# Optimization experiments

Measured on AMD Instinct MI355X. Metric: run time of the kernel, lower is better.

Reference implementation:

```python
import jax, jax.numpy as jnp
import numpy as np

N = 8192
TOKEN_DIM = 384
K = 16
D_IN = 2 * (TOKEN_DIM + 3)  # 774


def setup_inputs() -> dict:
    key = jax.random.key(0)
    k1, k2, k3, k4, k5, k6 = jax.random.split(key, 6)
    xyz = jax.random.normal(k1, (N, 3), dtype=jnp.float32)
    feat = jax.random.normal(k2, (N, TOKEN_DIM), dtype=jnp.float32)
    W1 = jax.random.normal(k3, (D_IN, TOKEN_DIM), dtype=jnp.float32) / np.sqrt(D_IN)
    b1 = jax.random.normal(k4, (TOKEN_DIM,), dtype=jnp.float32) * 0.01
    W2 = jax.random.normal(k5, (TOKEN_DIM, 3), dtype=jnp.float32) / np.sqrt(TOKEN_DIM)
    b2 = jax.random.normal(k6, (3,), dtype=jnp.float32) * 0.01
    return {"xyz": xyz, "feat": feat, "W1": W1, "b1": b1, "W2": W2, "b2": b2}


def _knn_idx(xyz, k):
    # pairwise squared distances [N, N]; loop=False -> exclude self via +inf diag
    sq = jnp.sum(xyz * xyz, axis=-1)
    d2 = sq[:, None] + sq[None, :] - 2.0 * (xyz @ xyz.T)
    n = xyz.shape[0]
    d2 = jnp.where(jnp.eye(n, dtype=bool), jnp.inf, d2)
    _, idx = jax.lax.top_k(-d2, k)  # idx[i] = k nearest neighbors (sources) of target i
    return idx


def reference(xyz, feat, W1, b1, W2, b2):
    idx = _knn_idx(xyz, K)                      # [N, K] int32
    x = jnp.concatenate([feat, xyz], axis=-1)   # [N, D] with D = token_dim + 3
    x_j = x[idx]                                # [N, K, D] gathered neighbor feats
    x_i = x[:, None, :]                         # [N, 1, D]
    # EdgeConv message: nn(cat([x_i, x_j - x_i]))
    e = jnp.concatenate([jnp.broadcast_to(x_i, x_j.shape), x_j - x_i], axis=-1)  # [N, K, 2D]
    h = jax.nn.relu(jnp.einsum('nkd,df->nkf', e, W1) + b1)   # [N, K, token_dim]
    m = jnp.einsum('nkf,fo->nko', h, W2) + b2                # [N, K, 3]
    agg = jnp.max(m, axis=1)                                 # max aggregation over neighbors
    return xyz + agg
```

## Files before the change

kernel.cpp:

```cpp
#include <hip/hip_runtime.h>
#include <hip/hip_bf16.h>


#define N 8192
#define TD 384
#define KNN 16
#define DX 387
#define KP 416
#define NF 768
#define INFF __builtin_inff()

#define NB_X (N/2)
#define NB_W NF
#define NB_A 32
#define NGEMM_T 1536

typedef __attribute__((ext_vector_type(8))) short short8;
typedef __attribute__((ext_vector_type(4))) float f32x4;
typedef __attribute__((ext_vector_type(2))) float f32x2;


__device__ __forceinline__ f32x2 pk_mul(f32x2 a, f32x2 b) {
    f32x2 r; asm("v_pk_mul_f32 %0, %1, %2" : "=v"(r) : "v"(a), "v"(b)); return r;
}
__device__ __forceinline__ f32x2 pk_add(f32x2 a, f32x2 b) {
    f32x2 r; asm("v_pk_add_f32 %0, %1, %2" : "=v"(r) : "v"(a), "v"(b)); return r;
}
__device__ __forceinline__ f32x2 pk_sub(f32x2 a, f32x2 b) {
    f32x2 r; asm("v_pk_add_f32 %0, %1, %2 neg_lo:[0,1] neg_hi:[0,1]" : "=v"(r) : "v"(a), "v"(b)); return r;
}
__device__ __forceinline__ f32x2 pk_fma(f32x2 a, f32x2 b, f32x2 c) {
    f32x2 r; asm("v_pk_fma_f32 %0, %1, %2, %3" : "=v"(r) : "v"(a), "v"(b), "v"(c)); return r;
}

__device__ __forceinline__ void dist4(f32x2 qx, f32x2 qy, f32x2 qz, f32x2 qw,
                                      f32x2 x01, f32x2 x23, f32x2 y01, f32x2 y23,
                                      f32x2 z01, f32x2 z23, f32x2 s01, f32x2 s23,
                                      f32x2& d01, f32x2& d23) {
    f32x2 dot01 = pk_fma(qz, z01, pk_fma(qy, y01, pk_mul(qx, x01)));
    f32x2 dot23 = pk_fma(qz, z23, pk_fma(qy, y23, pk_mul(qx, x23)));
    d01 = pk_sub(pk_add(qw, s01), pk_add(dot01, dot01));
    d23 = pk_sub(pk_add(qw, s23), pk_add(dot23, dot23));
}

__device__ __forceinline__ int xbin(float x) {
    int b = (int)((x + 4.0f) * 32.0f);
    return b < 0 ? 0 : (b > 255 ? 255 : b);
}

__device__ __forceinline__ float rdlane_f(float v, int src) {
    return __uint_as_float(__builtin_amdgcn_readlane(__float_as_uint(v), src));
}
__device__ __forceinline__ unsigned udmap(float x) {
    unsigned u = __float_as_uint(x);
    return ((int)u < 0) ? ~u : (u | 0x80000000u);
}


__global__ void __launch_bounds__(256) prep_assign(const float* __restrict__ feat,
                                                   const float* __restrict__ xyz,
                                                   const float* __restrict__ W1,
                                                   __hip_bfloat16* __restrict__ Xb,
                                                   __hip_bfloat16* __restrict__ Wpt,
                                                   int* __restrict__ tlo,
                                                   int* __restrict__ thi,
                                                   float* __restrict__ stile) {
    const int b = blockIdx.x;
    const int t = threadIdx.x;
    if (b < NB_X) {
        const int half = t >> 7;
        const int tt = t & 127;
        const int p = b*2 + half;
        if (tt < 96) {
            float4 f = reinterpret_cast<const float4*>(feat + (size_t)p*TD)[tt];
            __hip_bfloat16 h[4] = {__float2bfloat16(f.x), __float2bfloat16(f.y),
                                   __float2bfloat16(f.z), __float2bfloat16(f.w)};
            *reinterpret_cast<ulonglong1*>(Xb + p*KP + tt*4) = *reinterpret_cast<ulonglong1*>(h);
        } else {
            int d = TD + (tt - 96);
            float v = (d < DX) ? xyz[p*3 + (d - TD)] : 0.f;
            Xb[p*KP + d] = __float2bfloat16(v);
        }
        return;
    }
    if (b < NB_X + NB_W) {
        const int f = b - NB_X;
        for (int k = t; k < KP; k += 256) {
            float v = 0.f;
            if (k < DX) {
                if (f < TD) v = W1[k*TD + f] - W1[(DX+k)*TD + f];
                else        v = W1[(DX+k)*TD + (f - TD)];
            }
            Wpt[f*KP + k] = __float2bfloat16(v);
        }
        return;
    }

    __shared__ int hcnt[256], pre[256], scan[256], cur[256];
    __shared__ int stlo[32], sthi[32];
    const int a = b - (NB_X + NB_W);
    hcnt[t] = 0; pre[t] = 0; cur[t] = 0;
    if (t < 32) { stlo[t] = 255; sthi[t] = 0; }
    __syncthreads();

    #pragma unroll
    for (int c = 0; c < 32; ++c) {
        int bin = xbin(xyz[(c*256 + t)*3]);
        atomicAdd(&hcnt[bin], 1);
        if (c < a) atomicAdd(&pre[bin], 1);
    }
    __syncthreads();

    const int v = hcnt[t];
    scan[t] = v;
    __syncthreads();
    for (int off = 1; off < 256; off <<= 1) {
        int add = (t >= off) ? scan[t - off] : 0;
        __syncthreads();
        scan[t] += add;
        __syncthreads();
    }
    const int end = scan[t], start = end - v;
    if (a == 0 && v > 0) {
        for (int x = start >> 8; x <= (end - 1) >> 8; ++x) {
            atomicMin(&stlo[x], t);
            atomicMax(&sthi[x], t);
        }
    }
    __syncthreads();
    scan[t] = start;
    __syncthreads();
    if (a == 0 && t < 32) { tlo[t] = stlo[t]; thi[t] = sthi[t]; }

    const int i = a*256 + t;
    float x = xyz[i*3+0], y = xyz[i*3+1], z = xyz[i*3+2];
    int bin = xbin(x);
    int pos = scan[bin] + pre[bin] + atomicAdd(&cur[bin], 1);
    float sq = __fadd_rn(__fadd_rn(__fmul_rn(x,x), __fmul_rn(y,y)), __fmul_rn(z,z));
    float* tp = stile + (pos >> 8) * 1280 + (pos & 255);
    tp[0] = x; tp[256] = y; tp[512] = z; tp[768] = sq;
    reinterpret_cast<int*>(tp)[1024] = i;
}


__global__ void __launch_bounds__(64) knn_gemm(const float* __restrict__ stile,
                                               const int* __restrict__ tlo,
                                               const int* __restrict__ thi,
                                               int* __restrict__ knn,
                                               const __hip_bfloat16* __restrict__ Xb,
                                               const __hip_bfloat16* __restrict__ Wpt,
                                               const float* __restrict__ b1,
                                               __hip_bfloat16* __restrict__ Ub,
                                               __hip_bfloat16* __restrict__ Vb) {
    __shared__ unsigned sbuf[128][2];
    const int u = blockIdx.x;
    const int g = u / 6;
    const int r = u - g*6;
    const int lane = threadIdx.x;

    if ((r == 5) && (g < NGEMM_T)) {
        const int i0  = (g & 127) * 64;
        const int f0  = (g >> 7) * 64;
        const int lm  = lane & 15;
        const int lk  = (lane >> 4) * 8;

        f32x4 acc[4][4];
        #pragma unroll
        for (int rr = 0; rr < 4; ++rr)
            #pragma unroll
            for (int c = 0; c < 4; ++c)
                acc[rr][c] = (f32x4){0.f, 0.f, 0.f, 0.f};

        const __hip_bfloat16* xbase = Xb  + (size_t)(i0 + lm) * KP + lk;
        const __hip_bfloat16* wbase = Wpt + (size_t)(f0 + lm) * KP + lk;

        #pragma unroll
        for (int kk = 0; kk < 13; ++kk) {
            short8 aa[4], bb[4];
            #pragma unroll
            for (int rr = 0; rr < 4; ++rr)
                aa[rr] = *reinterpret_cast<const short8*>(xbase + (size_t)rr*16*KP + kk*32);
            #pragma unroll
            for (int c = 0; c < 4; ++c)
                bb[c] = *reinterpret_cast<const short8*>(wbase + (size_t)c*16*KP + kk*32);
            #pragma unroll
            for (int rr = 0; rr < 4; ++rr)
                #pragma unroll
                for (int c = 0; c < 4; ++c)
                    acc[rr][c] = __builtin_amdgcn_mfma_f32_16x16x32_bf16(aa[rr], bb[c], acc[rr][c], 0, 0, 0);
        }

        const bool isU = (f0 < TD);
        __hip_bfloat16* outb = isU ? (Ub + f0) : (Vb + (f0 - TD));
        float bias[4] = {0.f, 0.f, 0.f, 0.f};
        if (isU) {
            #pragma unroll
            for (int c = 0; c < 4; ++c) bias[c] = b1[f0 + c*16 + lm];
        }
        const int crow = (lane >> 4) * 4;
        #pragma unroll
        for (int rr = 0; rr < 4; ++rr)
            #pragma unroll
            for (int c = 0; c < 4; ++c)
                #pragma unroll
                for (int q = 0; q < 4; ++q)
                    outb[(size_t)(i0 + rr*16 + crow + q) * TD + c*16 + lm] =
                        __float2bfloat16(acc[rr][c][q] + bias[c]);
        return;
    }

    const int s  = u - ((g < NGEMM_T) ? g : NGEMM_T);
    const int tq   = s >> 8;
    const int sl   = (s & 255) >> 2;
    const int slot = s & 3;

    const float* qp = stile + tq*1280 + (s & 255);
    const float qx = qp[0], qy = qp[256], qz = qp[512], qw = qp[768];
    const int   qi = reinterpret_cast<const int*>(qp)[1024];
    const f32x2 qx2 = {qx,qx}, qy2 = {qy,qy}, qz2 = {qz,qz}, qw2 = {qw,qw};

    const float* lbase = stile + lane*4;
    const bool is_self_lane = (lane == sl);

    int lo = tq - 2; if (lo < 0) lo = 0; if (lo > 27) lo = 27;
    float4 X[5], Y[5], Z[5], S[5];
    int4   I[5];
    #pragma unroll
    for (int tt = 0; tt < 5; ++tt) {
        const float* tp = lbase + (lo + tt)*1280;
        X[tt] = *(const float4*)(tp);
        Y[tt] = *(const float4*)(tp + 256);
        Z[tt] = *(const float4*)(tp + 512);
        S[tt] = *(const float4*)(tp + 768);
        I[tt] = *(const int4*)(tp + 1024);
    }
    __builtin_amdgcn_sched_barrier(0);

    float dd[5][4];
    float mn = INFF;
    #pragma unroll
    for (int tt = 0; tt < 5; ++tt) {
        const int t = lo + tt;
        f32x2 x01 = {X[tt].x, X[tt].y}, x23 = {X[tt].z, X[tt].w};
        f32x2 y01 = {Y[tt].x, Y[tt].y}, y23 = {Y[tt].z, Y[tt].w};
        f32x2 z01 = {Z[tt].x, Z[tt].y}, z23 = {Z[tt].z, Z[tt].w};
        f32x2 s01 = {S[tt].x, S[tt].y}, s23 = {S[tt].z, S[tt].w};
        f32x2 d01, d23;
        dist4(qx2, qy2, qz2, qw2, x01, x23, y01, y23, z01, z23, s01, s23, d01, d23);
        if ((t == tq) && is_self_lane) {
            if      (slot == 0) d01[0] = INFF;
            else if (slot == 1) d01[1] = INFF;
            else if (slot == 2) d23[0] = INFF;
            else                d23[1] = INFF;
        }
        dd[tt][0] = d01[0]; dd[tt][1] = d01[1];
        dd[tt][2] = d23[0]; dd[tt][3] = d23[1];
        mn = fminf(mn, fminf(fminf(d01[0], d01[1]), fminf(d23[0], d23[1])));
    }

    float T;
    {
        unsigned ub = udmap(mn);
        unsigned long long alive = ~0ull;
        int need = KNN;
        for (int b = 31; b >= 0; --b) {
            if (__popcll(alive) == 1) break;
            unsigned long long ones  = __ballot(((ub >> b) & 1u) != 0u);
            unsigned long long zeros = alive & ~ones;
            int cz = (int)__popcll(zeros);
            bool tz = (cz >= need);
            alive = tz ? zeros : (alive & ones);
            need  = tz ? need : (need - cz);
        }
        T = fmaxf(rdlane_f(mn, (int)__ffsll(alive) - 1), 0.f);
    }

    unsigned mask;
    {
        const int ti = lane & 31;
        const int bl = tlo[ti], bh = thi[ti];
        const float xlo = (bl == 0)   ? -1e30f : (bl * 0.03125f - 4.0f);
        const float xhi = (bh == 255) ?  1e30f : ((bh + 1) * 0.03125f - 4.0f);
        float gap = fmaxf(0.f, fmaxf(xlo - qx, qx - xhi));
        bool gate = (gap * gap <= T + 1e-3f);
        mask = (unsigned)__ballot(gate && (lane < 32));
    }

    int cnt = 0;
    const unsigned long long ltm = (1ull << lane) - 1;

    auto push = [&](float dv, int idx) {
        bool pred = (dv <= T);
        unsigned long long bal = __ballot(pred);
        if (bal) {
            int posn = cnt + (int)__popcll(bal & ltm);
            if (pred && posn < 128) {
                sbuf[posn][0] = udmap(dv);
                sbuf[posn][1] = (unsigned)idx;
            }
            cnt += (int)__popcll(bal);
        }
    };

    #pragma unroll
    for (int tt = 0; tt < 5; ++tt) {
        const int t = lo + tt;
        if (!((mask >> t) & 1u)) continue;
        push(dd[tt][0], I[tt].x);
        push(dd[tt][1], I[tt].y);
        push(dd[tt][2], I[tt].z);
        push(dd[tt][3], I[tt].w);
    }
    unsigned rest = mask & ~(0x1Fu << lo);
    while (rest) {
        const int t = (int)__ffs(rest) - 1;
        rest &= rest - 1;
        const float* tp = lbase + t*1280;
        float4 Xr = *(const float4*)(tp);
        float4 Yr = *(const float4*)(tp + 256);
        float4 Zr = *(const float4*)(tp + 512);
        float4 Sr = *(const float4*)(tp + 768);
        int4   Ir = *(const int4*)(tp + 1024);
        f32x2 x01 = {Xr.x,Xr.y}, x23 = {Xr.z,Xr.w};
        f32x2 y01 = {Yr.x,Yr.y}, y23 = {Yr.z,Yr.w};
        f32x2 z01 = {Zr.x,Zr.y}, z23 = {Zr.z,Zr.w};
        f32x2 s01 = {Sr.x,Sr.y}, s23 = {Sr.z,Sr.w};
        f32x2 d01, d23;
        dist4(qx2, qy2, qz2, qw2, x01, x23, y01, y23, z01, z23, s01, s23, d01, d23);
        float tmin = fminf(fminf(d01[0], d01[1]), fminf(d23[0], d23[1]));
        if (__ballot(tmin <= T)) {
            push(d01[0], Ir.x);
            push(d01[1], Ir.y);
            push(d23[0], Ir.z);
            push(d23[1], Ir.w);
        }
    }

    asm volatile("s_waitcnt lgkmcnt(0)" ::: "memory");
    const int M = (cnt > 128) ? 128 : cnt;

    if (M <= 64) {
        unsigned ud1 = 0xFFFFFFFFu, id1 = 0xFFFFFFFFu;
        if (lane < M) { ud1 = sbuf[lane][0]; id1 = sbuf[lane][1]; }
        unsigned long long alive = __ballot(lane < M);
        int need = KNN;
        for (int b = 31; b >= 0; --b) {
            if (__popcll(alive) == 1) break;
            unsigned long long on = __ballot(((ud1 >> b) & 1u) != 0u);
            unsigned long long z  = alive & ~on;
            int cz = (int)__popcll(z);
            bool tz = (cz >= need);
            alive = tz ? z : (alive & on);
            need  = tz ? need : (need - cz);
        }
        unsigned v16 = (unsigned)__builtin_amdgcn_readlane((int)ud1, (int)__ffsll(alive) - 1);
        const bool all_ties = ((int)__popcll(alive) <= need);
        unsigned vidx = 0xFFFFFFFFu;
        if (!all_ties) {
            unsigned long long a = alive;
            int nd = need;
            for (int b = 31; b >= 0; --b) {
                if (__popcll(a) == 1) break;
                unsigned long long on = __ballot(((id1 >> b) & 1u) != 0u);
                unsigned long long z  = a & ~on;
                int cz = (int)__popcll(z);
                bool tz = (cz >= nd);
                a  = tz ? z : (a & on);
                nd = tz ? nd : (nd - cz);
            }
            vidx = (unsigned)__builtin_amdgcn_readlane((int)id1, (int)__ffsll(a) - 1);
        }
        bool sel = (lane < M) && ((ud1 < v16) || ((ud1 == v16) && (all_ties || (id1 <= vidx))));
        unsigned long long bs = __ballot(sel);
        if (sel) knn[qi*KNN + (int)__popcll(bs & ltm)] = (int)id1;
    } else {
        unsigned ud1 = 0xFFFFFFFFu, id1 = 0xFFFFFFFFu;
        unsigned ud2 = 0xFFFFFFFFu, id2 = 0xFFFFFFFFu;
        if (lane < M)      { ud1 = sbuf[lane][0];      id1 = sbuf[lane][1]; }
        if (lane + 64 < M) { ud2 = sbuf[lane + 64][0]; id2 = sbuf[lane + 64][1]; }

        unsigned long long alive1 = __ballot(lane < M);
        unsigned long long alive2 = __ballot(lane + 64 < M);
        int need = KNN;
        for (int b = 31; b >= 0; --b) {
            if ((int)__popcll(alive1) + (int)__popcll(alive2) == 1) break;
            unsigned long long on1 = __ballot(((ud1 >> b) & 1u) != 0u);
            unsigned long long on2 = __ballot(((ud2 >> b) & 1u) != 0u);
            unsigned long long z1 = alive1 & ~on1;
            unsigned long long z2 = alive2 & ~on2;
            int cz = (int)__popcll(z1) + (int)__popcll(z2);
            bool tz = (cz >= need);
            alive1 = tz ? z1 : (alive1 & on1);
            alive2 = tz ? z2 : (alive2 & on2);
            need   = tz ? need : (need - cz);
        }
        unsigned v16;
        if (alive1) v16 = (unsigned)__builtin_amdgcn_readlane((int)ud1, (int)__ffsll(alive1) - 1);
        else        v16 = (unsigned)__builtin_amdgcn_readlane((int)ud2, (int)__ffsll(alive2) - 1);

        const int nt = (int)__popcll(alive1) + (int)__popcll(alive2);
        const bool all_ties = (nt <= need);
        unsigned vidx = 0xFFFFFFFFu;
        if (!all_ties) {
            unsigned long long a1 = alive1, a2 = alive2;
            int nd = need;
            for (int b = 31; b >= 0; --b) {
                if ((int)__popcll(a1) + (int)__popcll(a2) == 1) break;
                unsigned long long on1 = __ballot(((id1 >> b) & 1u) != 0u);
                unsigned long long on2 = __ballot(((id2 >> b) & 1u) != 0u);
                unsigned long long z1 = a1 & ~on1;
                unsigned long long z2 = a2 & ~on2;
                int cz = (int)__popcll(z1) + (int)__popcll(z2);
                bool tz = (cz >= nd);
                a1 = tz ? z1 : (a1 & on1);
                a2 = tz ? z2 : (a2 & on2);
                nd = tz ? nd : (nd - cz);
            }
            if (a1) vidx = (unsigned)__builtin_amdgcn_readlane((int)id1, (int)__ffsll(a1) - 1);
            else    vidx = (unsigned)__builtin_amdgcn_readlane((int)id2, (int)__ffsll(a2) - 1);
        }

        bool sel1 = (lane < M)      && ((ud1 < v16) || ((ud1 == v16) && (all_ties || (id1 <= vidx))));
        bool sel2 = (lane + 64 < M) && ((ud2 < v16) || ((ud2 == v16) && (all_ties || (id2 <= vidx))));
        unsigned long long bs1 = __ballot(sel1);
        if (sel1) knn[qi*KNN + (int)__popcll(bs1 & ltm)] = (int)id1;
        const int c1 = (int)__popcll(bs1);
        unsigned long long bs2 = __ballot(sel2);
        if (sel2) knn[qi*KNN + c1 + (int)__popcll(bs2 & ltm)] = (int)id2;
    }
}


__device__ __forceinline__ float bflo(unsigned w) { return __uint_as_float(w << 16); }
__device__ __forceinline__ float bfhi(unsigned w) { return __uint_as_float(w & 0xFFFF0000u); }

template<int CTRL>
__device__ __forceinline__ float dppf(float v) {
    return __uint_as_float((unsigned)__builtin_amdgcn_update_dpp(
        0, (int)__float_as_uint(v), CTRL, 0xF, 0xF, true));
}

__global__ void __launch_bounds__(256) final_kernel(const __hip_bfloat16* __restrict__ Ub,
                                                    const __hip_bfloat16* __restrict__ Vb,
                                                    const int* __restrict__ knn,
                                                    const float* __restrict__ xyz,
                                                    const float* __restrict__ W2,
                                                    const float* __restrict__ b2,
                                                    float* __restrict__ out) {
    const int lane = threadIdx.x & 63;
    const int wv   = threadIdx.x >> 6;
    const int i    = blockIdx.x * 4 + wv;
    const int d0   = lane * 6;

    int jreg = knn[i*KNN + (lane & 15)];

    float u[6], w2l[6][3];
    {
        const unsigned* rowU = reinterpret_cast<const unsigned*>(Ub + (size_t)i * TD) + lane*3;
        unsigned a0 = rowU[0], a1 = rowU[1], a2 = rowU[2];
        u[0] = bflo(a0); u[1] = bfhi(a0);
        u[2] = bflo(a1); u[3] = bfhi(a1);
        u[4] = bflo(a2); u[5] = bfhi(a2);
    }
    #pragma unroll
    for (int t = 0; t < 6; ++t)
        #pragma unroll
        for (int c = 0; c < 3; ++c) w2l[t][c] = W2[(d0 + t)*3 + c];

    const unsigned* vbase = reinterpret_cast<const unsigned*>(Vb);
    const int voff = lane * 3;

    float pk0[16], pk1[16], pk2[16];
    unsigned va[2][4][3];

    #pragma unroll
    for (int t = 0; t < 4; ++t) {
        int j = __builtin_amdgcn_readlane(jreg, t);
        const unsigned* rv = vbase + (size_t)j * 192 + voff;
        va[0][t][0] = rv[0]; va[0][t][1] = rv[1]; va[0][t][2] = rv[2];
    }
    __builtin_amdgcn_sched_barrier(0);

    #pragma unroll
    for (int b = 0; b < 4; ++b) {
        if (b < 3) {
            #pragma unroll
            for (int t = 0; t < 4; ++t) {
                int j = __builtin_amdgcn_readlane(jreg, (b+1)*4 + t);
                const unsigned* rv = vbase + (size_t)j * 192 + voff;
                va[(b+1)&1][t][0] = rv[0];
                va[(b+1)&1][t][1] = rv[1];
                va[(b+1)&1][t][2] = rv[2];
            }
            __builtin_amdgcn_sched_barrier(0);
        }
        #pragma unroll
        for (int t = 0; t < 4; ++t) {
            const int kk = b*4 + t;
            unsigned a0 = va[b&1][t][0], a1 = va[b&1][t][1], a2 = va[b&1][t][2];
            float v0 = bflo(a0), v1 = bfhi(a0);
            float v2 = bflo(a1), v3 = bfhi(a1);
            float v4 = bflo(a2), v5 = bfhi(a2);
            float h0 = fmaxf(u[0] + v0, 0.f), h1 = fmaxf(u[1] + v1, 0.f);
            float h2 = fmaxf(u[2] + v2, 0.f), h3 = fmaxf(u[3] + v3, 0.f);
            float h4 = fmaxf(u[4] + v4, 0.f), h5 = fmaxf(u[5] + v5, 0.f);
            float s0 = 0.f, s1 = 0.f, s2 = 0.f;
            s0 = fmaf(h0, w2l[0][0], s0); s1 = fmaf(h0, w2l[0][1], s1); s2 = fmaf(h0, w2l[0][2], s2);
            s0 = fmaf(h1, w2l[1][0], s0); s1 = fmaf(h1, w2l[1][1], s1); s2 = fmaf(h1, w2l[1][2], s2);
            s0 = fmaf(h2, w2l[2][0], s0); s1 = fmaf(h2, w2l[2][1], s1); s2 = fmaf(h2, w2l[2][2], s2);
            s0 = fmaf(h3, w2l[3][0], s0); s1 = fmaf(h3, w2l[3][1], s1); s2 = fmaf(h3, w2l[3][2], s2);
            s0 = fmaf(h4, w2l[4][0], s0); s1 = fmaf(h4, w2l[4][1], s1); s2 = fmaf(h4, w2l[4][2], s2);
            s0 = fmaf(h5, w2l[5][0], s0); s1 = fmaf(h5, w2l[5][1], s1); s2 = fmaf(h5, w2l[5][2], s2);
            pk0[kk] = s0; pk1[kk] = s1; pk2[kk] = s2;
        }
    }

    #pragma unroll
    for (int kk = 0; kk < 16; ++kk) {
        float r0 = pk0[kk], r1 = pk1[kk], r2 = pk2[kk];
        r0 += dppf<0x121>(r0); r1 += dppf<0x121>(r1); r2 += dppf<0x121>(r2);
        r0 += dppf<0x122>(r0); r1 += dppf<0x122>(r1); r2 += dppf<0x122>(r2);
        r0 += dppf<0x124>(r0); r1 += dppf<0x124>(r1); r2 += dppf<0x124>(r2);
        r0 += dppf<0x128>(r0); r1 += dppf<0x128>(r1); r2 += dppf<0x128>(r2);
        r0 += __shfl_xor(r0, 16); r1 += __shfl_xor(r1, 16); r2 += __shfl_xor(r2, 16);
        r0 += __shfl_xor(r0, 32); r1 += __shfl_xor(r1, 32); r2 += __shfl_xor(r2, 32);
        pk0[kk] = r0; pk1[kk] = r1; pk2[kk] = r2;
    }
    float mx0 = pk0[0], mx1 = pk1[0], mx2 = pk2[0];
    #pragma unroll
    for (int kk = 1; kk < 16; ++kk) {
        mx0 = fmaxf(mx0, pk0[kk]);
        mx1 = fmaxf(mx1, pk1[kk]);
        mx2 = fmaxf(mx2, pk2[kk]);
    }

    if (lane == 0) {
        out[i*3+0] = xyz[i*3+0] + mx0 + b2[0];
        out[i*3+1] = xyz[i*3+1] + mx1 + b2[1];
        out[i*3+2] = xyz[i*3+2] + mx2 + b2[2];
    }
}


extern "C" void kernel_launch(void* const* d_in, const int* in_sizes, int n_in,
                              void* d_out, int out_size, void* d_ws, size_t ws_size,
                              hipStream_t stream) {
    const float* xyz  = (const float*)d_in[0];
    const float* feat = (const float*)d_in[1];
    const float* W1   = (const float*)d_in[2];
    const float* b1   = (const float*)d_in[3];
    const float* W2   = (const float*)d_in[4];
    const float* b2   = (const float*)d_in[5];
    float* out = (float*)d_out;

    char* ws = (char*)d_ws;
    int*            knn   = (int*)(ws + 0);
    float*          stile = (float*)(ws + 524288);
    __hip_bfloat16* Xb    = (__hip_bfloat16*)(ws + 688128);
    __hip_bfloat16* Wpt   = (__hip_bfloat16*)(ws + 7503872);
    __hip_bfloat16* Ub    = (__hip_bfloat16*)(ws + 8142848);
    __hip_bfloat16* Vb    = (__hip_bfloat16*)(ws + 14434304);
    int*            thi   = (int*)(ws + 20725760);
    int*            tlo   = (int*)(ws + 20725888);

    prep_assign <<<dim3(NB_X + NB_W + NB_A), dim3(256), 0, stream>>>(
        feat, xyz, W1, Xb, Wpt, tlo, thi, stile);
    knn_gemm    <<<dim3(N + NGEMM_T),        dim3(64),  0, stream>>>(
        stile, tlo, thi, knn, Xb, Wpt, b1, Ub, Vb);
    final_kernel<<<dim3(N/4),                dim3(256), 0, stream>>>(
        Ub, Vb, knn, xyz, W2, b2, out);
}
```

Before: 78.84 us.

## Process four KNN queries per wavefront to reuse candidate tile loads

Each 64-lane KNN block now handles four consecutive queries instead of one. The candidate tiles are loaded once and shared across the four queries, and the ballot-based radix selects are interleaved across queries. The grid interleave changes from 5 KNN blocks plus 1 GEMM block to 4 KNN plus 3 GEMM per group of seven. In exchange, register pressure rises with per-query state arrays, distances are recomputed in the push phase, the early-exit shortcuts in the selects are dropped, and far tiles are gated with the union of the four queries' thresholds.

```diff
diff --git a/kernel.cpp b/kernel.cpp
--- a/kernel.cpp
+++ b/kernel.cpp
@@ -13,6 +13,7 @@
 #define NB_X (N/2)
 #define NB_W NF
 #define NB_A 32
+#define NKNN_B 2048
 #define NGEMM_T 1536
 
 typedef __attribute__((ext_vector_type(8))) short short8;
@@ -152,17 +153,18 @@
                                                const float* __restrict__ b1,
                                                __hip_bfloat16* __restrict__ Ub,
                                                __hip_bfloat16* __restrict__ Vb) {
-    __shared__ unsigned sbuf[128][2];
+    __shared__ unsigned sbuf[4][128][2];
     const int u = blockIdx.x;
-    const int g = u / 6;
-    const int r = u - g*6;
+    const int sep = u / 7;
+    const int rem = u - sep*7;
     const int lane = threadIdx.x;
 
-    if ((r == 5) && (g < NGEMM_T)) {
-        const int i0  = (g & 127) * 64;
-        const int f0  = (g >> 7) * 64;
-        const int lm  = lane & 15;
-        const int lk  = (lane >> 4) * 8;
+    if (rem >= 4) {
+        const int g  = sep*3 + (rem - 4);
+        const int i0 = (g & 127) * 64;
+        const int f0 = (g >> 7) * 64;
+        const int lm = lane & 15;
+        const int lk = (lane >> 4) * 8;
 
         f32x4 acc[4][4];
         #pragma unroll
@@ -209,15 +211,31 @@
         return;
     }
 
-    const int s  = u - ((g < NGEMM_T) ? g : NGEMM_T);
-    const int tq   = s >> 8;
-    const int sl   = (s & 255) >> 2;
-    const int slot = s & 3;
-
-    const float* qp = stile + tq*1280 + (s & 255);
-    const float qx = qp[0], qy = qp[256], qz = qp[512], qw = qp[768];
-    const int   qi = reinterpret_cast<const int*>(qp)[1024];
-    const f32x2 qx2 = {qx,qx}, qy2 = {qy,qy}, qz2 = {qz,qz}, qw2 = {qw,qw};
+    const int kb = sep*4 + rem;
+    const int s0 = kb * 4;
+    const int tq = s0 >> 8;
+    const int sl = (s0 & 255) >> 2;
+
+    const float* qp = stile + tq*1280 + (s0 & 255);
+    float4 QX = *(const float4*)(qp);
+    float4 QY = *(const float4*)(qp + 256);
+    float4 QZ = *(const float4*)(qp + 512);
+    float4 QW = *(const float4*)(qp + 768);
+    int4   QI = *(const int4*)(qp + 1024);
+    const float qxa[4] = {QX.x, QX.y, QX.z, QX.w};
+    const int   qia[4] = {QI.x, QI.y, QI.z, QI.w};
+    f32x2 qx2[4], qy2[4], qz2[4], qw2[4];
+    {
+        float qya[4] = {QY.x,QY.y,QY.z,QY.w};
+        float qza[4] = {QZ.x,QZ.y,QZ.z,QZ.w}, qwa[4] = {QW.x,QW.y,QW.z,QW.w};
+        #pragma unroll
+        for (int q = 0; q < 4; ++q) {
+            qx2[q] = (f32x2){qxa[q], qxa[q]};
+            qy2[q] = (f32x2){qya[q], qya[q]};
+            qz2[q] = (f32x2){qza[q], qza[q]};
+            qw2[q] = (f32x2){qwa[q], qwa[q]};
+        }
+    }
 
     const float* lbase = stile + lane*4;
     const bool is_self_lane = (lane == sl);
@@ -236,8 +254,7 @@
     }
     __builtin_amdgcn_sched_barrier(0);
 
-    float dd[5][4];
-    float mn = INFF;
+    float mn[4] = {INFF, INFF, INFF, INFF};
     #pragma unroll
     for (int tt = 0; tt < 5; ++tt) {
         const int t = lo + tt;
@@ -245,35 +262,45 @@
         f32x2 y01 = {Y[tt].x, Y[tt].y}, y23 = {Y[tt].z, Y[tt].w};
         f32x2 z01 = {Z[tt].x, Z[tt].y}, z23 = {Z[tt].z, Z[tt].w};
         f32x2 s01 = {S[tt].x, S[tt].y}, s23 = {S[tt].z, S[tt].w};
-        f32x2 d01, d23;
-        dist4(qx2, qy2, qz2, qw2, x01, x23, y01, y23, z01, z23, s01, s23, d01, d23);
-        if ((t == tq) && is_self_lane) {
-            if      (slot == 0) d01[0] = INFF;
-            else if (slot == 1) d01[1] = INFF;
-            else if (slot == 2) d23[0] = INFF;
-            else                d23[1] = INFF;
-        }
-        dd[tt][0] = d01[0]; dd[tt][1] = d01[1];
-        dd[tt][2] = d23[0]; dd[tt][3] = d23[1];
-        mn = fminf(mn, fminf(fminf(d01[0], d01[1]), fminf(d23[0], d23[1])));
-    }
-
-    float T;
+        const bool selft = (t == tq) && is_self_lane;
+        #pragma unroll
+        for (int q = 0; q < 4; ++q) {
+            f32x2 d01, d23;
+            dist4(qx2[q], qy2[q], qz2[q], qw2[q],
+                  x01, x23, y01, y23, z01, z23, s01, s23, d01, d23);
+            if (selft) {
+                if      (q == 0) d01[0] = INFF;
+                else if (q == 1) d01[1] = INFF;
+                else if (q == 2) d23[0] = INFF;
+                else             d23[1] = INFF;
+            }
+            mn[q] = fminf(mn[q], fminf(fminf(d01[0], d01[1]), fminf(d23[0], d23[1])));
+        }
+    }
+
+    float T[4];
     {
-        unsigned ub = udmap(mn);
-        unsigned long long alive = ~0ull;
-        int need = KNN;
+        unsigned ub[4];
+        unsigned long long alive[4];
+        int need[4];
+        #pragma unroll
+        for (int q = 0; q < 4; ++q) { ub[q] = udmap(mn[q]); alive[q] = ~0ull; need[q] = KNN; }
         for (int b = 31; b >= 0; --b) {
-            if (__popcll(alive) == 1) break;
-            unsigned long long ones  = __ballot(((ub >> b) & 1u) != 0u);
-            unsigned long long zeros = alive & ~ones;
-            int cz = (int)__popcll(zeros);
-            bool tz = (cz >= need);
-            alive = tz ? zeros : (alive & ones);
-            need  = tz ? need : (need - cz);
-        }
-        T = fmaxf(rdlane_f(mn, (int)__ffsll(alive) - 1), 0.f);
-    }
+            #pragma unroll
+            for (int q = 0; q < 4; ++q) {
+                unsigned long long ones  = __ballot(((ub[q] >> b) & 1u) != 0u);
+                unsigned long long zeros = alive[q] & ~ones;
+                int cz = (int)__popcll(zeros);
+                bool tz = (cz >= need[q]);
+                alive[q] = tz ? zeros : (alive[q] & ones);
+                need[q]  = tz ? need[q] : (need[q] - cz);
+            }
+        }
+        #pragma unroll
+        for (int q = 0; q < 4; ++q)
+            T[q] = fmaxf(rdlane_f(mn[q], (int)__ffsll(alive[q]) - 1), 0.f);
+    }
+    const float Tmax = fmaxf(fmaxf(T[0], T[1]), fmaxf(T[2], T[3]));
 
     unsigned mask;
     {
@@ -281,24 +308,28 @@
         const int bl = tlo[ti], bh = thi[ti];
         const float xlo = (bl == 0)   ? -1e30f : (bl * 0.03125f - 4.0f);
         const float xhi = (bh == 255) ?  1e30f : ((bh + 1) * 0.03125f - 4.0f);
-        float gap = fmaxf(0.f, fmaxf(xlo - qx, qx - xhi));
-        bool gate = (gap * gap <= T + 1e-3f);
+        bool gate = false;
+        #pragma unroll
+        for (int q = 0; q < 4; ++q) {
+            float gap = fmaxf(0.f, fmaxf(xlo - qxa[q], qxa[q] - xhi));
+            gate = gate || (gap * gap <= T[q] + 1e-3f);
+        }
         mask = (unsigned)__ballot(gate && (lane < 32));
     }
 
-    int cnt = 0;
+    int cnt[4] = {0, 0, 0, 0};
     const unsigned long long ltm = (1ull << lane) - 1;
 
-    auto push = [&](float dv, int idx) {
-        bool pred = (dv <= T);
+    auto push = [&](int q, float dv, int idx) {
+        bool pred = (dv <= T[q]);
         unsigned long long bal = __ballot(pred);
         if (bal) {
-            int posn = cnt + (int)__popcll(bal & ltm);
+            int posn = cnt[q] + (int)__popcll(bal & ltm);
             if (pred && posn < 128) {
-                sbuf[posn][0] = udmap(dv);
-                sbuf[posn][1] = (unsigned)idx;
-            }
-            cnt += (int)__popcll(bal);
+                sbuf[q][posn][0] = udmap(dv);
+                sbuf[q][posn][1] = (unsigned)idx;
+            }
+            cnt[q] += (int)__popcll(bal);
         }
     };
 
@@ -306,10 +337,27 @@
     for (int tt = 0; tt < 5; ++tt) {
         const int t = lo + tt;
         if (!((mask >> t) & 1u)) continue;
-        push(dd[tt][0], I[tt].x);
-        push(dd[tt][1], I[tt].y);
-        push(dd[tt][2], I[tt].z);
-        push(dd[tt][3], I[tt].w);
+        f32x2 x01 = {X[tt].x, X[tt].y}, x23 = {X[tt].z, X[tt].w};
+        f32x2 y01 = {Y[tt].x, Y[tt].y}, y23 = {Y[tt].z, Y[tt].w};
+        f32x2 z01 = {Z[tt].x, Z[tt].y}, z23 = {Z[tt].z, Z[tt].w};
+        f32x2 s01 = {S[tt].x, S[tt].y}, s23 = {S[tt].z, S[tt].w};
+        const bool selft = (t == tq) && is_self_lane;
+        #pragma unroll
+        for (int q = 0; q < 4; ++q) {
+            f32x2 d01, d23;
+            dist4(qx2[q], qy2[q], qz2[q], qw2[q],
+                  x01, x23, y01, y23, z01, z23, s01, s23, d01, d23);
+            if (selft) {
+                if      (q == 0) d01[0] = INFF;
+                else if (q == 1) d01[1] = INFF;
+                else if (q == 2) d23[0] = INFF;
+                else             d23[1] = INFF;
+            }
+            push(q, d01[0], I[tt].x);
+            push(q, d01[1], I[tt].y);
+            push(q, d23[0], I[tt].z);
+            push(q, d23[1], I[tt].w);
+        }
     }
     unsigned rest = mask & ~(0x1Fu << lo);
     while (rest) {
@@ -325,108 +373,87 @@
         f32x2 y01 = {Yr.x,Yr.y}, y23 = {Yr.z,Yr.w};
         f32x2 z01 = {Zr.x,Zr.y}, z23 = {Zr.z,Zr.w};
         f32x2 s01 = {Sr.x,Sr.y}, s23 = {Sr.z,Sr.w};
-        f32x2 d01, d23;
-        dist4(qx2, qy2, qz2, qw2, x01, x23, y01, y23, z01, z23, s01, s23, d01, d23);
-        float tmin = fminf(fminf(d01[0], d01[1]), fminf(d23[0], d23[1]));
-        if (__ballot(tmin <= T)) {
-            push(d01[0], Ir.x);
-            push(d01[1], Ir.y);
-            push(d23[0], Ir.z);
-            push(d23[1], Ir.w);
+        #pragma unroll
+        for (int q = 0; q < 4; ++q) {
+            f32x2 d01, d23;
+            dist4(qx2[q], qy2[q], qz2[q], qw2[q],
+                  x01, x23, y01, y23, z01, z23, s01, s23, d01, d23);
+            float tmin = fminf(fminf(d01[0], d01[1]), fminf(d23[0], d23[1]));
+            if (__ballot(tmin <= Tmax)) {
+                push(q, d01[0], Ir.x);
+                push(q, d01[1], Ir.y);
+                push(q, d23[0], Ir.z);
+                push(q, d23[1], Ir.w);
+            }
         }
     }
 
     asm volatile("s_waitcnt lgkmcnt(0)" ::: "memory");
-    const int M = (cnt > 128) ? 128 : cnt;
-
-    if (M <= 64) {
-        unsigned ud1 = 0xFFFFFFFFu, id1 = 0xFFFFFFFFu;
-        if (lane < M) { ud1 = sbuf[lane][0]; id1 = sbuf[lane][1]; }
-        unsigned long long alive = __ballot(lane < M);
-        int need = KNN;
-        for (int b = 31; b >= 0; --b) {
-            if (__popcll(alive) == 1) break;
-            unsigned long long on = __ballot(((ud1 >> b) & 1u) != 0u);
-            unsigned long long z  = alive & ~on;
-            int cz = (int)__popcll(z);
-            bool tz = (cz >= need);
-            alive = tz ? z : (alive & on);
-            need  = tz ? need : (need - cz);
-        }
-        unsigned v16 = (unsigned)__builtin_amdgcn_readlane((int)ud1, (int)__ffsll(alive) - 1);
-        const bool all_ties = ((int)__popcll(alive) <= need);
+    int M[4];
+    unsigned ud1[4], id1[4], ud2[4], id2[4];
+    unsigned long long a1[4], a2[4];
+    int need[4];
+    #pragma unroll
+    for (int q = 0; q < 4; ++q) {
+        M[q] = (cnt[q] > 128) ? 128 : cnt[q];
+        ud1[q] = 0xFFFFFFFFu; id1[q] = 0xFFFFFFFFu;
+        ud2[q] = 0xFFFFFFFFu; id2[q] = 0xFFFFFFFFu;
+        if (lane < M[q])      { ud1[q] = sbuf[q][lane][0];      id1[q] = sbuf[q][lane][1]; }
+        if (lane + 64 < M[q]) { ud2[q] = sbuf[q][lane + 64][0]; id2[q] = sbuf[q][lane + 64][1]; }
+        a1[q] = __ballot(lane < M[q]);
+        a2[q] = __ballot(lane + 64 < M[q]);
+        need[q] = KNN;
+    }
+    for (int b = 31; b >= 0; --b) {
+        #pragma unroll
+        for (int q = 0; q < 4; ++q) {
+            unsigned long long on1 = __ballot(((ud1[q] >> b) & 1u) != 0u);
+            unsigned long long on2 = __ballot(((ud2[q] >> b) & 1u) != 0u);
+            unsigned long long z1 = a1[q] & ~on1;
+            unsigned long long z2 = a2[q] & ~on2;
+            int cz = (int)__popcll(z1) + (int)__popcll(z2);
+            bool tz = (cz >= need[q]);
+            a1[q]   = tz ? z1 : (a1[q] & on1);
+            a2[q]   = tz ? z2 : (a2[q] & on2);
+            need[q] = tz ? need[q] : (need[q] - cz);
+        }
+    }
+
+    #pragma unroll
+    for (int q = 0; q < 4; ++q) {
+        unsigned v16;
+        if (a1[q]) v16 = (unsigned)__builtin_amdgcn_readlane((int)ud1[q], (int)__ffsll(a1[q]) - 1);
+        else       v16 = (unsigned)__builtin_amdgcn_readlane((int)ud2[q], (int)__ffsll(a2[q]) - 1);
+
+        const int nt = (int)__popcll(a1[q]) + (int)__popcll(a2[q]);
+        const bool all_ties = (nt <= need[q]);
         unsigned vidx = 0xFFFFFFFFu;
         if (!all_ties) {
-            unsigned long long a = alive;
-            int nd = need;
+            unsigned long long b1m = a1[q], b2m = a2[q];
+            int nd = need[q];
             for (int b = 31; b >= 0; --b) {
-                if (__popcll(a) == 1) break;
-                unsigned long long on = __ballot(((id1 >> b) & 1u) != 0u);
-                unsigned long long z  = a & ~on;
-                int cz = (int)__popcll(z);
-                bool tz = (cz >= nd);
-                a  = tz ? z : (a & on);
-                nd = tz ? nd : (nd - cz);
-            }
-            vidx = (unsigned)__builtin_amdgcn_readlane((int)id1, (int)__ffsll(a) - 1);
-        }
-        bool sel = (lane < M) && ((ud1 < v16) || ((ud1 == v16) && (all_ties || (id1 <= vidx))));
-        unsigned long long bs = __ballot(sel);
-        if (sel) knn[qi*KNN + (int)__popcll(bs & ltm)] = (int)id1;
-    } else {
-        unsigned ud1 = 0xFFFFFFFFu, id1 = 0xFFFFFFFFu;
-        unsigned ud2 = 0xFFFFFFFFu, id2 = 0xFFFFFFFFu;
-        if (lane < M)      { ud1 = sbuf[lane][0];      id1 = sbuf[lane][1]; }
-        if (lane + 64 < M) { ud2 = sbuf[lane + 64][0]; id2 = sbuf[lane + 64][1]; }
-
-        unsigned long long alive1 = __ballot(lane < M);
-        unsigned long long alive2 = __ballot(lane + 64 < M);
-        int need = KNN;
-        for (int b = 31; b >= 0; --b) {
-            if ((int)__popcll(alive1) + (int)__popcll(alive2) == 1) break;
-            unsigned long long on1 = __ballot(((ud1 >> b) & 1u) != 0u);
-            unsigned long long on2 = __ballot(((ud2 >> b) & 1u) != 0u);
-            unsigned long long z1 = alive1 & ~on1;
-            unsigned long long z2 = alive2 & ~on2;
-            int cz = (int)__popcll(z1) + (int)__popcll(z2);
-            bool tz = (cz >= need);
-            alive1 = tz ? z1 : (alive1 & on1);
-            alive2 = tz ? z2 : (alive2 & on2);
-            need   = tz ? need : (need - cz);
-        }
-        unsigned v16;
-        if (alive1) v16 = (unsigned)__builtin_amdgcn_readlane((int)ud1, (int)__ffsll(alive1) - 1);
-        else        v16 = (unsigned)__builtin_amdgcn_readlane((int)ud2, (int)__ffsll(alive2) - 1);
-
-        const int nt = (int)__popcll(alive1) + (int)__popcll(alive2);
-        const bool all_ties = (nt <= need);
-        unsigned vidx = 0xFFFFFFFFu;
-        if (!all_ties) {
-            unsigned long long a1 = alive1, a2 = alive2;
-            int nd = need;
-            for (int b = 31; b >= 0; --b) {
-                if ((int)__popcll(a1) + (int)__popcll(a2) == 1) break;
-                unsigned long long on1 = __ballot(((id1 >> b) & 1u) != 0u);
-                unsigned long long on2 = __ballot(((id2 >> b) & 1u) != 0u);
-                unsigned long long z1 = a1 & ~on1;
-                unsigned long long z2 = a2 & ~on2;
+                if ((int)__popcll(b1m) + (int)__popcll(b2m) == 1) break;
+                unsigned long long on1 = __ballot(((id1[q] >> b) & 1u) != 0u);
+                unsigned long long on2 = __ballot(((id2[q] >> b) & 1u) != 0u);
+                unsigned long long z1 = b1m & ~on1;
+                unsigned long long z2 = b2m & ~on2;
                 int cz = (int)__popcll(z1) + (int)__popcll(z2);
                 bool tz = (cz >= nd);
-                a1 = tz ? z1 : (a1 & on1);
-                a2 = tz ? z2 : (a2 & on2);
-                nd = tz ? nd : (nd - cz);
-            }
-            if (a1) vidx = (unsigned)__builtin_amdgcn_readlane((int)id1, (int)__ffsll(a1) - 1);
-            else    vidx = (unsigned)__builtin_amdgcn_readlane((int)id2, (int)__ffsll(a2) - 1);
-        }
-
-        bool sel1 = (lane < M)      && ((ud1 < v16) || ((ud1 == v16) && (all_ties || (id1 <= vidx))));
-        bool sel2 = (lane + 64 < M) && ((ud2 < v16) || ((ud2 == v16) && (all_ties || (id2 <= vidx))));
+                b1m = tz ? z1 : (b1m & on1);
+                b2m = tz ? z2 : (b2m & on2);
+                nd  = tz ? nd : (nd - cz);
+            }
+            if (b1m) vidx = (unsigned)__builtin_amdgcn_readlane((int)id1[q], (int)__ffsll(b1m) - 1);
+            else     vidx = (unsigned)__builtin_amdgcn_readlane((int)id2[q], (int)__ffsll(b2m) - 1);
+        }
+
+        bool sel1 = (lane < M[q])      && ((ud1[q] < v16) || ((ud1[q] == v16) && (all_ties || (id1[q] <= vidx))));
+        bool sel2 = (lane + 64 < M[q]) && ((ud2[q] < v16) || ((ud2[q] == v16) && (all_ties || (id2[q] <= vidx))));
         unsigned long long bs1 = __ballot(sel1);
-        if (sel1) knn[qi*KNN + (int)__popcll(bs1 & ltm)] = (int)id1;
+        if (sel1) knn[qia[q]*KNN + (int)__popcll(bs1 & ltm)] = (int)id1[q];
         const int c1 = (int)__popcll(bs1);
         unsigned long long bs2 = __ballot(sel2);
-        if (sel2) knn[qi*KNN + c1 + (int)__popcll(bs2 & ltm)] = (int)id2;
+        if (sel2) knn[qia[q]*KNN + c1 + (int)__popcll(bs2 & ltm)] = (int)id2[q];
     }
 }
 
@@ -563,10 +590,10 @@
     int*            thi   = (int*)(ws + 20725760);
     int*            tlo   = (int*)(ws + 20725888);
 
-    prep_assign <<<dim3(NB_X + NB_W + NB_A), dim3(256), 0, stream>>>(
+    prep_assign <<<dim3(NB_X + NB_W + NB_A),  dim3(256), 0, stream>>>(
         feat, xyz, W1, Xb, Wpt, tlo, thi, stile);
-    knn_gemm    <<<dim3(N + NGEMM_T),        dim3(64),  0, stream>>>(
+    knn_gemm    <<<dim3(NKNN_B + NGEMM_T),    dim3(64),  0, stream>>>(
         stile, tlo, thi, knn, Xb, Wpt, b1, Ub, Vb);
-    final_kernel<<<dim3(N/4),                dim3(256), 0, stream>>>(
+    final_kernel<<<dim3(N/4),                 dim3(256), 0, stream>>>(
         Ub, Vb, knn, xyz, W2, b2, out);
 }
```

New measurement: 92.16 us. 16.9% more time.

## Replace ballot radix-select with LDS rank counting and atomic candidate compaction

Applied to the files above, without the earlier changes.

Swaps the bitwise ballot radix-select used for the threshold and the final top-16 selection for a rank-counting scheme, where each lane counts how many LDS entries are smaller than its own value. Candidate compaction now uses an LDS atomicAdd counter instead of ballot/popcount prefix sums, and the per-tile early-out ballot is dropped. The goal is to remove long serial ballot chains. In exchange it adds O(M) LDS reads per lane and atomic contention. Output order within a row now follows rank rather than buffer order.

```diff
diff --git a/kernel.cpp b/kernel.cpp
--- a/kernel.cpp
+++ b/kernel.cpp
@@ -153,6 +153,8 @@
                                                __hip_bfloat16* __restrict__ Ub,
                                                __hip_bfloat16* __restrict__ Vb) {
     __shared__ unsigned sbuf[128][2];
+    __shared__ float    tbuf[64];
+    __shared__ int      scnt;
     const int u = blockIdx.x;
     const int g = u / 6;
     const int r = u - g*6;
@@ -260,19 +262,18 @@
 
     float T;
     {
-        unsigned ub = udmap(mn);
-        unsigned long long alive = ~0ull;
-        int need = KNN;
-        for (int b = 31; b >= 0; --b) {
-            if (__popcll(alive) == 1) break;
-            unsigned long long ones  = __ballot(((ub >> b) & 1u) != 0u);
-            unsigned long long zeros = alive & ~ones;
-            int cz = (int)__popcll(zeros);
-            bool tz = (cz >= need);
-            alive = tz ? zeros : (alive & ones);
-            need  = tz ? need : (need - cz);
-        }
-        T = fmaxf(rdlane_f(mn, (int)__ffsll(alive) - 1), 0.f);
+        tbuf[lane] = mn;
+        if (lane == 0) scnt = 0;
+        asm volatile("s_waitcnt lgkmcnt(0)" ::: "memory");
+        __builtin_amdgcn_sched_barrier(0);
+        int trank = 0;
+        #pragma unroll 8
+        for (int j = 0; j < 64; ++j) {
+            float v = tbuf[j];
+            trank += ((v < mn) || (v == mn && j < lane)) ? 1 : 0;
+        }
+        unsigned long long bt = __ballot(trank == 15);
+        T = fmaxf(rdlane_f(mn, (int)__ffsll(bt) - 1), 0.f);
     }
 
     unsigned mask;
@@ -286,19 +287,13 @@
         mask = (unsigned)__ballot(gate && (lane < 32));
     }
 
-    int cnt = 0;
-    const unsigned long long ltm = (1ull << lane) - 1;
-
     auto push = [&](float dv, int idx) {
-        bool pred = (dv <= T);
-        unsigned long long bal = __ballot(pred);
-        if (bal) {
-            int posn = cnt + (int)__popcll(bal & ltm);
-            if (pred && posn < 128) {
-                sbuf[posn][0] = udmap(dv);
-                sbuf[posn][1] = (unsigned)idx;
+        if (dv <= T) {
+            int pos = atomicAdd(&scnt, 1);
+            if (pos < 128) {
+                sbuf[pos][0] = udmap(dv);
+                sbuf[pos][1] = (unsigned)idx;
             }
-            cnt += (int)__popcll(bal);
         }
     };
 
@@ -327,107 +322,31 @@
         f32x2 s01 = {Sr.x,Sr.y}, s23 = {Sr.z,Sr.w};
         f32x2 d01, d23;
         dist4(qx2, qy2, qz2, qw2, x01, x23, y01, y23, z01, z23, s01, s23, d01, d23);
-        float tmin = fminf(fminf(d01[0], d01[1]), fminf(d23[0], d23[1]));
-        if (__ballot(tmin <= T)) {
-            push(d01[0], Ir.x);
-            push(d01[1], Ir.y);
-            push(d23[0], Ir.z);
-            push(d23[1], Ir.w);
-        }
+        push(d01[0], Ir.x);
+        push(d01[1], Ir.y);
+        push(d23[0], Ir.z);
+        push(d23[1], Ir.w);
     }
 
     asm volatile("s_waitcnt lgkmcnt(0)" ::: "memory");
-    const int M = (cnt > 128) ? 128 : cnt;
-
-    if (M <= 64) {
-        unsigned ud1 = 0xFFFFFFFFu, id1 = 0xFFFFFFFFu;
-        if (lane < M) { ud1 = sbuf[lane][0]; id1 = sbuf[lane][1]; }
-        unsigned long long alive = __ballot(lane < M);
-        int need = KNN;
-        for (int b = 31; b >= 0; --b) {
-            if (__popcll(alive) == 1) break;
-            unsigned long long on = __ballot(((ud1 >> b) & 1u) != 0u);
-            unsigned long long z  = alive & ~on;
-            int cz = (int)__popcll(z);
-            bool tz = (cz >= need);
-            alive = tz ? z : (alive & on);
-            need  = tz ? need : (need - cz);
-        }
-        unsigned v16 = (unsigned)__builtin_amdgcn_readlane((int)ud1, (int)__ffsll(alive) - 1);
-        const bool all_ties = ((int)__popcll(alive) <= need);
-        unsigned vidx = 0xFFFFFFFFu;
-        if (!all_ties) {
-            unsigned long long a = alive;
-            int nd = need;
-            for (int b = 31; b >= 0; --b) {
-                if (__popcll(a) == 1) break;
-                unsigned long long on = __ballot(((id1 >> b) & 1u) != 0u);
-                unsigned long long z  = a & ~on;
-                int cz = (int)__popcll(z);
-                bool tz = (cz >= nd);
-                a  = tz ? z : (a & on);
-                nd = tz ? nd : (nd - cz);
-            }
-            vidx = (unsigned)__builtin_amdgcn_readlane((int)id1, (int)__ffsll(a) - 1);
-        }
-        bool sel = (lane < M) && ((ud1 < v16) || ((ud1 == v16) && (all_ties || (id1 <= vidx))));
-        unsigned long long bs = __ballot(sel);
-        if (sel) knn[qi*KNN + (int)__popcll(bs & ltm)] = (int)id1;
-    } else {
-        unsigned ud1 = 0xFFFFFFFFu, id1 = 0xFFFFFFFFu;
-        unsigned ud2 = 0xFFFFFFFFu, id2 = 0xFFFFFFFFu;
-        if (lane < M)      { ud1 = sbuf[lane][0];      id1 = sbuf[lane][1]; }
-        if (lane + 64 < M) { ud2 = sbuf[lane + 64][0]; id2 = sbuf[lane + 64][1]; }
-
-        unsigned long long alive1 = __ballot(lane < M);
-        unsigned long long alive2 = __ballot(lane + 64 < M);
-        int need = KNN;
-        for (int b = 31; b >= 0; --b) {
-            if ((int)__popcll(alive1) + (int)__popcll(alive2) == 1) break;
-            unsigned long long on1 = __ballot(((ud1 >> b) & 1u) != 0u);
-            unsigned long long on2 = __ballot(((ud2 >> b) & 1u) != 0u);
-            unsigned long long z1 = alive1 & ~on1;
-            unsigned long long z2 = alive2 & ~on2;
-            int cz = (int)__popcll(z1) + (int)__popcll(z2);
-            bool tz = (cz >= need);
-            alive1 = tz ? z1 : (alive1 & on1);
-            alive2 = tz ? z2 : (alive2 & on2);
-            need   = tz ? need : (need - cz);
-        }
-        unsigned v16;
-        if (alive1) v16 = (unsigned)__builtin_amdgcn_readlane((int)ud1, (int)__ffsll(alive1) - 1);
-        else        v16 = (unsigned)__builtin_amdgcn_readlane((int)ud2, (int)__ffsll(alive2) - 1);
-
-        const int nt = (int)__popcll(alive1) + (int)__popcll(alive2);
-        const bool all_ties = (nt <= need);
-        unsigned vidx = 0xFFFFFFFFu;
-        if (!all_ties) {
-            unsigned long long a1 = alive1, a2 = alive2;
-            int nd = need;
-            for (int b = 31; b >= 0; --b) {
-                if ((int)__popcll(a1) + (int)__popcll(a2) == 1) break;
-                unsigned long long on1 = __ballot(((id1 >> b) & 1u) != 0u);
-                unsigned long long on2 = __ballot(((id2 >> b) & 1u) != 0u);
-                unsigned long long z1 = a1 & ~on1;
-                unsigned long long z2 = a2 & ~on2;
-                int cz = (int)__popcll(z1) + (int)__popcll(z2);
-                bool tz = (cz >= nd);
-                a1 = tz ? z1 : (a1 & on1);
-                a2 = tz ? z2 : (a2 & on2);
-                nd = tz ? nd : (nd - cz);
-            }
-            if (a1) vidx = (unsigned)__builtin_amdgcn_readlane((int)id1, (int)__ffsll(a1) - 1);
-            else    vidx = (unsigned)__builtin_amdgcn_readlane((int)id2, (int)__ffsll(a2) - 1);
-        }
-
-        bool sel1 = (lane < M)      && ((ud1 < v16) || ((ud1 == v16) && (all_ties || (id1 <= vidx))));
-        bool sel2 = (lane + 64 < M) && ((ud2 < v16) || ((ud2 == v16) && (all_ties || (id2 <= vidx))));
-        unsigned long long bs1 = __ballot(sel1);
-        if (sel1) knn[qi*KNN + (int)__popcll(bs1 & ltm)] = (int)id1;
-        const int c1 = (int)__popcll(bs1);
-        unsigned long long bs2 = __ballot(sel2);
-        if (sel2) knn[qi*KNN + c1 + (int)__popcll(bs2 & ltm)] = (int)id2;
-    }
+    __builtin_amdgcn_sched_barrier(0);
+    int M = scnt;
+    if (M > 128) M = 128;
+
+    unsigned ud1 = 0xFFFFFFFFu, id1 = 0xFFFFFFFFu;
+    unsigned ud2 = 0xFFFFFFFFu, id2 = 0xFFFFFFFFu;
+    if (lane < M)      { ud1 = sbuf[lane][0];      id1 = sbuf[lane][1]; }
+    if (lane + 64 < M) { ud2 = sbuf[lane + 64][0]; id2 = sbuf[lane + 64][1]; }
+
+    int r1 = 0, r2 = 0;
+    for (int j = 0; j < M; ++j) {
+        unsigned uj = sbuf[j][0];
+        unsigned ij = sbuf[j][1];
+        r1 += ((uj < ud1) || (uj == ud1 && ij < id1)) ? 1 : 0;
+        r2 += ((uj < ud2) || (uj == ud2 && ij < id2)) ? 1 : 0;
+    }
+    if (lane < M && r1 < KNN)        knn[qi*KNN + r1] = (int)id1;
+    if (lane + 64 < M && r2 < KNN)   knn[qi*KNN + r2] = (int)id2;
 }
 
 
```

Measured after the change: 82.84 us. +5.1%, slower.
